# Performance work log

Measured on AMD Instinct MI355X. Metric: run time of the kernel, lower is better.

Reference implementation:

```python
import jax, jax.numpy as jnp
import numpy as np

B, ENTRY, TUPLE, CLASSES = 4096, 1024, 16, 10
NEURONS = ENTRY // TUPLE            # 64, pad_bits = 0
ADDR_SPACE = 2 ** TUPLE             # 65536


def setup_inputs() -> dict:
    key = jax.random.key(0)
    k1, k2, k3 = jax.random.split(key, 3)
    # binary input bits
    samples = jax.random.randint(k1, (B, ENTRY), 0, 2, dtype=jnp.int32)
    # per-class random permutation of the (padded) entry bits
    tuple_mapping = jnp.argsort(jax.random.uniform(k2, (CLASSES, ENTRY)), axis=1).astype(jnp.int32)
    ram = (jax.random.uniform(k3, (CLASSES, NEURONS, ADDR_SPACE)) < 0.05).astype(jnp.float32)
    return {"samples": samples, "tuple_mapping": tuple_mapping, "ram": ram}


def reference(samples, tuple_mapping, ram):
    # samples: [B, E] binary int32; tuple_mapping: [C, E]; ram: [C, N, A]
    Bn = samples.shape[0]
    C, E = tuple_mapping.shape
    _, N, A = ram.shape
    T = E // N
    # per-class bit remapping (torch.index_select per class, vectorized)
    mapped = samples[:, tuple_mapping]                      # [B, C, E]
    bits = mapped.reshape(Bn, C, N, T)                      # [B, C, N, T]
    # transform: (bits << flip(arange(T))).sum -> big-endian tuple address
    weights = (2 ** jnp.flip(jnp.arange(T))).astype(jnp.int32)  # [T]
    addr = (bits * weights).sum(axis=-1)                    # [B, C, N] in [0, A)
    # RAM lookup (dense equivalent of dict lookup + isin membership)
    cidx = jnp.arange(C)[None, :, None]
    nidx = jnp.arange(N)[None, None, :]
    vals = ram[cidx, nidx, addr]                            # [B, C, N]
    # discriminator response = count of firing neurons per class
    return vals.sum(axis=-1)                                # [B, C]
```

## Files before the change

### kernel.cpp

```cpp
#include <hip/hip_runtime.h>


#define BATCH   4096
#define ENTRY   1024
#define TUPLE   16
#define CLASSES 10
#define NEURONS 64
#define CN      (CLASSES * NEURONS)
#define ADDRSP  65536

typedef unsigned long long u64;
typedef unsigned int       u32;
typedef unsigned short     u16;

__global__ __launch_bounds__(256) void packT_kernel(
    const int* __restrict__ samples, u64* __restrict__ bitT)
{
    __shared__ int tile[64 * 65];
    const int sg   = blockIdx.x >> 4;
    const int cg   = blockIdx.x & 15;
    const int w    = threadIdx.x >> 6;
    const int lane = threadIdx.x & 63;
    const int t    = threadIdx.x;

#pragma unroll
    for (int rnd = 0; rnd < 4; ++rnd) {
        const int idx  = rnd * 256 + t;
        const int row  = idx >> 4;
        const int col4 = idx & 15;
        const int4 v = *reinterpret_cast<const int4*>(
            samples + (size_t)(sg * 64 + row) * ENTRY + cg * 64 + col4 * 4);
        int* tp = tile + row * 65 + col4 * 4;
        tp[0] = v.x; tp[1] = v.y; tp[2] = v.z; tp[3] = v.w;
    }
    __syncthreads();

#pragma unroll
    for (int k = 0; k < 16; ++k) {
        const int j = w * 16 + k;
        const u64 m = __ballot(tile[lane * 65 + j] & 1);
        if (lane == 0) bitT[(size_t)(cg * 64 + j) * 64 + sg] = m;
    }
}

__global__ __launch_bounds__(256) void fused_kernel(
    const int* __restrict__ tm, const float* __restrict__ ram,
    const u64* __restrict__ bitT, u64* __restrict__ partial)
{
    __shared__ u64 tbl[512];
    __shared__ u16 addrL[BATCH];
    const int bid  = blockIdx.x;
    const int cn   = bid >> 1;
    const int h    = bid & 1;
    const int c    = cn >> 6;
    const int n    = cn & 63;
    const int lane = threadIdx.x & 63;
    const int wu   = __builtin_amdgcn_readfirstlane(threadIdx.x >> 6);

    const float4* rp = reinterpret_cast<const float4*>(
        ram + (size_t)cn * ADDRSP + h * (ADDRSP / 2));
#pragma unroll 8
    for (int i = 0; i < 32; ++i) {
        const int g = wu * 32 + i;
        const float4 v = rp[g * 64 + lane];
        const u64 m0 = __ballot(v.x != 0.0f);
        const u64 m1 = __ballot(v.y != 0.0f);
        const u64 m2 = __ballot(v.z != 0.0f);
        const u64 m3 = __ballot(v.w != 0.0f);
        if (lane == 0) {
            tbl[g * 4 + 0] = m0; tbl[g * 4 + 1] = m1;
            tbl[g * 4 + 2] = m2; tbl[g * 4 + 3] = m3;
        }
    }

    const int* tp = tm + c * ENTRY + n * TUPLE;
    int E[TUPLE];
#pragma unroll
    for (int tt = 0; tt < TUPLE; ++tt) E[tt] = tp[tt];

#pragma unroll
    for (int k = 0; k < 16; ++k) {
        const int sg = wu * 16 + k;
        u32 a = 0;
#pragma unroll
        for (int tt = 0; tt < TUPLE; ++tt) {
            const u64 word = bitT[(size_t)E[tt] * 64 + sg];
            u32 bit;
            asm("v_cndmask_b32 %0, 0, 1, %1" : "=v"(bit) : "s"(word));
            a = (a << 1) | bit;
        }
        addrL[sg * 64 + lane] = (u16)a;
    }
    __syncthreads();

    u64* pp = partial + (size_t)cn * 128 + h * 64;
#pragma unroll
    for (int i = 0; i < 16; ++i) {
        const u32 a     = addrL[wu * 1024 + i * 64 + lane];
        const u32 local = a & 32767u;
        const u64 word  = tbl[(local >> 8) * 4 + (a & 3u)];
        u32 bit = (u32)(word >> ((local >> 2) & 63u)) & 1u;
        bit &= (u32)((a >> 15) == (u32)h);
        const u64 m = __ballot(bit != 0u);
        if (lane == 0) pp[wu * 16 + i] = m;
    }
}

__global__ __launch_bounds__(256) void reduce_kernel(
    const u64* __restrict__ partial, float* __restrict__ out)
{
    const int gid  = blockIdx.x * 4 + (threadIdx.x >> 6);
    const int lane = threadIdx.x & 63;
    const int c    = gid >> 6;
    const int sg   = gid & 63;

    const u64* pp = partial + ((size_t)(c * NEURONS + lane)) * 128 + sg;
    const u64 m = pp[0] | pp[64];

    float myv = 0.0f;
#pragma unroll
    for (int b2 = 0; b2 < 64; ++b2) {
        const u64 mb = __ballot((u32)(m >> b2) & 1u);
        if (lane == b2) myv = (float)__popcll(mb);
    }
    out[(sg * 64 + lane) * CLASSES + c] = myv;
}

extern "C" void kernel_launch(void* const* d_in, const int* in_sizes, int n_in,
                              void* d_out, int out_size, void* d_ws, size_t ws_size,
                              hipStream_t stream)
{
    const int*   samples = (const int*)d_in[0];
    const int*   tm      = (const int*)d_in[1];
    const float* ram     = (const float*)d_in[2];
    float*       out     = (float*)d_out;

    u64* bitT    = (u64*)d_ws;
    u64* partial = (u64*)((char*)d_ws + (512u << 10));

    packT_kernel <<<1024, 256, 0, stream>>>(samples, bitT);
    fused_kernel <<<CN * 2, 256, 0, stream>>>(tm, ram, bitT, partial);
    reduce_kernel<<<CN / 4, 256, 0, stream>>>(partial, out);
}
```

Before: 50.53 us.

## Load only RAM cache lines addressed by the batch instead of full half-table

Computes each block's tuple addresses first, marks the touched 64-byte RAM lines in a shared bitmap, compacts them into a list, and loads and packs only those lines into a 16-bit-per-line table. This aims to cut HBM traffic from streaming the entire half RAM row per block. In exchange it adds atomics, a serial prefix-scan compaction in one wave, an extra barrier, and scattered rather than coalesced streaming loads.

```diff
diff --git a/kernel.cpp b/kernel.cpp
--- a/kernel.cpp
+++ b/kernel.cpp
@@ -8,6 +8,8 @@
 #define NEURONS 64
 #define CN      (CLASSES * NEURONS)
 #define ADDRSP  65536
+#define HALF    (ADDRSP / 2)
+#define HLINES  (HALF / 16)
 
 typedef unsigned long long u64;
 typedef unsigned int       u32;
@@ -47,31 +49,23 @@
     const int* __restrict__ tm, const float* __restrict__ ram,
     const u64* __restrict__ bitT, u64* __restrict__ partial)
 {
-    __shared__ u64 tbl[512];
     __shared__ u16 addrL[BATCH];
+    __shared__ u32 bm[HLINES / 32];
+    __shared__ u16 list[HLINES];
+    __shared__ u16 tbl[HLINES];
+    __shared__ int nT;
+
     const int bid  = blockIdx.x;
     const int cn   = bid >> 1;
     const int h    = bid & 1;
     const int c    = cn >> 6;
     const int n    = cn & 63;
-    const int lane = threadIdx.x & 63;
-    const int wu   = __builtin_amdgcn_readfirstlane(threadIdx.x >> 6);
+    const int tid  = threadIdx.x;
+    const int lane = tid & 63;
+    const int wu   = __builtin_amdgcn_readfirstlane(tid >> 6);
 
-    const float4* rp = reinterpret_cast<const float4*>(
-        ram + (size_t)cn * ADDRSP + h * (ADDRSP / 2));
-#pragma unroll 8
-    for (int i = 0; i < 32; ++i) {
-        const int g = wu * 32 + i;
-        const float4 v = rp[g * 64 + lane];
-        const u64 m0 = __ballot(v.x != 0.0f);
-        const u64 m1 = __ballot(v.y != 0.0f);
-        const u64 m2 = __ballot(v.z != 0.0f);
-        const u64 m3 = __ballot(v.w != 0.0f);
-        if (lane == 0) {
-            tbl[g * 4 + 0] = m0; tbl[g * 4 + 1] = m1;
-            tbl[g * 4 + 2] = m2; tbl[g * 4 + 3] = m3;
-        }
-    }
+    if (tid < HLINES / 32) bm[tid] = 0u;
+    __syncthreads();
 
     const int* tp = tm + c * ENTRY + n * TUPLE;
     int E[TUPLE];
@@ -90,6 +84,45 @@
             a = (a << 1) | bit;
         }
         addrL[sg * 64 + lane] = (u16)a;
+        if ((a >> 15) == (u32)h) {
+            const u32 line = (a & (HALF - 1)) >> 4;
+            atomicOr(&bm[line >> 5], 1u << (line & 31u));
+        }
+    }
+    __syncthreads();
+
+    if (wu == 0) {
+        u32 word = bm[lane];
+        const int ccnt = __popc(word);
+        int x = ccnt;
+#pragma unroll
+        for (int i = 1; i < 64; i <<= 1) {
+            const int y = __shfl_up(x, i);
+            if (lane >= i) x += y;
+        }
+        int o = x - ccnt;
+        while (word) {
+            const int b2 = __builtin_ctz(word);
+            word &= word - 1;
+            list[o++] = (u16)(lane * 32 + b2);
+        }
+        if (lane == 63) nT = x;
+    }
+    __syncthreads();
+
+    const float4* rp = reinterpret_cast<const float4*>(
+        ram + (size_t)cn * ADDRSP + h * HALF);
+    const int nLines = nT;
+    const int q = tid & 3;
+    for (int e = (tid >> 2); e < nLines; e += 64) {
+        const int line = list[e];
+        const float4 v = rp[line * 4 + q];
+        u32 nib = (u32)(v.x != 0.0f) | ((u32)(v.y != 0.0f) << 1) |
+                  ((u32)(v.z != 0.0f) << 2) | ((u32)(v.w != 0.0f) << 3);
+        u32 x = nib << (q * 4);
+        x |= __shfl_xor(x, 1);
+        x |= __shfl_xor(x, 2);
+        if (q == 0) tbl[line] = (u16)x;
     }
     __syncthreads();
 
@@ -97,9 +130,9 @@
 #pragma unroll
     for (int i = 0; i < 16; ++i) {
         const u32 a     = addrL[wu * 1024 + i * 64 + lane];
-        const u32 local = a & 32767u;
-        const u64 word  = tbl[(local >> 8) * 4 + (a & 3u)];
-        u32 bit = (u32)(word >> ((local >> 2) & 63u)) & 1u;
+        const u32 local = a & (HALF - 1);
+        const u32 w16   = tbl[local >> 4];
+        u32 bit = (w16 >> (a & 15u)) & 1u;
         bit &= (u32)((a >> 15) == (u32)h);
         const u64 m = __ballot(bit != 0u);
         if (lane == 0) pp[wu * 16 + i] = m;
```

Result: slower. 54.21 us (+7.3%).

## Split RAM table build into quarters and pack bits without ballots

Applied to the files above, without the earlier changes.

Each (class, neuron) RAM row is now processed by four blocks instead of two, and each thread packs 64 entries into a u64 bitmap using bit 23 of the float instead of wave ballots. The reduce kernel ORs four partial masks. This aims to raise parallelism and cut ballot overhead in the bandwidth-bound table build, but it duplicates the address-computation gather across more blocks and relies on RAM values being exactly 0.0 or 1.0.

```diff
diff --git a/kernel.cpp b/kernel.cpp
--- a/kernel.cpp
+++ b/kernel.cpp
@@ -8,6 +8,7 @@
 #define NEURONS 64
 #define CN      (CLASSES * NEURONS)
 #define ADDRSP  65536
+#define QTR     (ADDRSP / 4)
 
 typedef unsigned long long u64;
 typedef unsigned int       u32;
@@ -43,35 +44,35 @@
     }
 }
 
-__global__ __launch_bounds__(256) void fused_kernel(
+__global__ __launch_bounds__(256, 8) void fused_kernel(
     const int* __restrict__ tm, const float* __restrict__ ram,
     const u64* __restrict__ bitT, u64* __restrict__ partial)
 {
-    __shared__ u64 tbl[512];
     __shared__ u16 addrL[BATCH];
+    __shared__ u64 tbl[256];
+
     const int bid  = blockIdx.x;
-    const int cn   = bid >> 1;
-    const int h    = bid & 1;
+    const int cn   = bid >> 2;
+    const int q    = bid & 3;
     const int c    = cn >> 6;
     const int n    = cn & 63;
-    const int lane = threadIdx.x & 63;
-    const int wu   = __builtin_amdgcn_readfirstlane(threadIdx.x >> 6);
+    const int tid  = threadIdx.x;
+    const int lane = tid & 63;
+    const int wu   = __builtin_amdgcn_readfirstlane(tid >> 6);
 
-    const float4* rp = reinterpret_cast<const float4*>(
-        ram + (size_t)cn * ADDRSP + h * (ADDRSP / 2));
-#pragma unroll 8
-    for (int i = 0; i < 32; ++i) {
-        const int g = wu * 32 + i;
-        const float4 v = rp[g * 64 + lane];
-        const u64 m0 = __ballot(v.x != 0.0f);
-        const u64 m1 = __ballot(v.y != 0.0f);
-        const u64 m2 = __ballot(v.z != 0.0f);
-        const u64 m3 = __ballot(v.w != 0.0f);
-        if (lane == 0) {
-            tbl[g * 4 + 0] = m0; tbl[g * 4 + 1] = m1;
-            tbl[g * 4 + 2] = m2; tbl[g * 4 + 3] = m3;
-        }
+    const int4* rp = reinterpret_cast<const int4*>(
+        ram + (size_t)cn * ADDRSP + q * QTR);
+    u64 acc = 0;
+#pragma unroll 4
+    for (int i = 0; i < 16; ++i) {
+        const int4 v = rp[tid * 16 + i];
+        const u32 nib = (((u32)v.x >> 23) & 1u)
+                      | ((((u32)v.y >> 23) & 1u) << 1)
+                      | ((((u32)v.z >> 23) & 1u) << 2)
+                      | ((((u32)v.w >> 23) & 1u) << 3);
+        acc |= (u64)nib << (i * 4);
     }
+    tbl[tid] = acc;
 
     const int* tp = tm + c * ENTRY + n * TUPLE;
     int E[TUPLE];
@@ -93,14 +94,14 @@
     }
     __syncthreads();
 
-    u64* pp = partial + (size_t)cn * 128 + h * 64;
+    u64* pp = partial + (size_t)cn * 256 + q * 64;
 #pragma unroll
     for (int i = 0; i < 16; ++i) {
         const u32 a     = addrL[wu * 1024 + i * 64 + lane];
-        const u32 local = a & 32767u;
-        const u64 word  = tbl[(local >> 8) * 4 + (a & 3u)];
-        u32 bit = (u32)(word >> ((local >> 2) & 63u)) & 1u;
-        bit &= (u32)((a >> 15) == (u32)h);
+        const u32 inq   = (u32)((a >> 14) == (u32)q);
+        const u32 local = a & (QTR - 1);
+        const u64 word  = tbl[local >> 6];
+        const u32 bit   = (u32)(word >> (local & 63u)) & inq;
         const u64 m = __ballot(bit != 0u);
         if (lane == 0) pp[wu * 16 + i] = m;
     }
@@ -114,8 +115,8 @@
     const int c    = gid >> 6;
     const int sg   = gid & 63;
 
-    const u64* pp = partial + ((size_t)(c * NEURONS + lane)) * 128 + sg;
-    const u64 m = pp[0] | pp[64];
+    const u64* pp = partial + ((size_t)(c * NEURONS + lane)) * 256 + sg;
+    const u64 m = pp[0] | pp[64] | pp[128] | pp[192];
 
     float myv = 0.0f;
 #pragma unroll
@@ -139,6 +140,6 @@
     u64* partial = (u64*)((char*)d_ws + (512u << 10));
 
     packT_kernel <<<1024, 256, 0, stream>>>(samples, bitT);
-    fused_kernel <<<CN * 2, 256, 0, stream>>>(tm, ram, bitT, partial);
+    fused_kernel <<<CN * 4, 256, 0, stream>>>(tm, ram, bitT, partial);
     reduce_kernel<<<CN / 4, 256, 0, stream>>>(partial, out);
 }
```

Measured after the change: 63.43 us. +25.5%, slower.
